# Performance work log

Measured on AMD Instinct MI355X. Metric: run time of the kernel, lower is better.

Reference implementation:

```python
import jax, jax.numpy as jnp
import numpy as np

B, D, CL, QL = 32, 128, 1024, 512


def setup_inputs() -> dict:
    key = jax.random.key(0)
    kC, kQ, kW = jax.random.split(key, 3)
    C = jax.random.normal(kC, (B, D, CL), dtype=jnp.float32)
    Q = jax.random.normal(kQ, (B, D, QL), dtype=jnp.float32)
    # xavier_normal_ on (B*CL, 1, 3D): std = sqrt(2 / (fan_in + fan_out)) = sqrt(2/(1+3D))
    std = (2.0 / (1.0 + 3.0 * D)) ** 0.5
    W = jax.random.normal(kW, (B * CL, 1, 3 * D), dtype=jnp.float32) * std
    return {"C": C, "Q": Q, "W": W}


def reference(C, Q, W):
    # C: (B, D, CL), Q: (B, D, QL), W: (B*CL, 1, 3D)
    b, d, cl = C.shape
    Ct = jnp.transpose(C, (0, 2, 1))   # (B, CL, D)
    Qt = jnp.transpose(Q, (0, 2, 1))   # (B, QL, D)
    Wr = W.reshape(b, cl, 3 * d)
    wq, wc, wqc = Wr[..., :d], Wr[..., d:2 * d], Wr[..., 2 * d:]
    # Trilinear similarity: S[b,c,q] = wq[b,c].Q[b,q] + wc[b,c].C[b,c] + wqc[b,c].(C[b,c]*Q[b,q])
    S = (jnp.einsum('bcd,bqd->bcq', wq, Qt)
         + jnp.sum(wc * Ct, axis=-1, keepdims=True)
         + jnp.einsum('bcd,bqd->bcq', wqc * Ct, Qt))   # (B, CL, QL)
    S1 = jax.nn.softmax(S, axis=2)  # over queries
    S2 = jax.nn.softmax(S, axis=1)  # over context
    A = jnp.einsum('bcq,bqd->bcd', S1, Qt)             # (B, CL, D)
    # B = (S1 @ S2^T) @ C, reassociated as S1 @ (S2^T @ C) to avoid (CL,CL) intermediate
    S2tC = jnp.einsum('bkq,bkd->bqd', S2, Ct)          # (B, QL, D)
    Bm = jnp.einsum('bcq,bqd->bcd', S1, S2tC)          # (B, CL, D)
    out = jnp.concatenate([Ct, A, Ct * A, Ct * Bm], axis=2)  # (B, CL, 4D)
    # dropout is identity in eval mode
    return jnp.transpose(out, (0, 2, 1))               # (B, 4D, CL)
```

## Files before the change

kernel.cpp:

```cpp
#include <hip/hip_runtime.h>
#include <hip/hip_bf16.h>
#include <cstddef>

#define B_  32
#define D_  128
#define CL_ 1024
#define QL_ 512

using short8  = __attribute__((ext_vector_type(8))) short;
using short4v = __attribute__((ext_vector_type(4))) short;
using float4v = __attribute__((ext_vector_type(4))) float;

__device__ __forceinline__ unsigned short f2bf(float f) {
    unsigned int u = __float_as_uint(f);
    u += 0x7FFFu + ((u >> 16) & 1u);
    return (unsigned short)(u >> 16);
}
__device__ __forceinline__ float bf2f(unsigned short h) {
    return __uint_as_float(((unsigned int)h) << 16);
}

__global__ __launch_bounds__(256) void k_u_bias(const float* __restrict__ C,
                                                const float* __restrict__ W,
                                                unsigned short* __restrict__ U,
                                                float* __restrict__ bias,
                                                unsigned short* __restrict__ Cbf) {
    int b  = blockIdx.y;
    int c0 = blockIdx.x * 32;
    int tid = threadIdx.x;

    __shared__ float tile[128][33];
    __shared__ float bred[32][9];

    for (int pass = 0; pass < 16; ++pass) {
        int d = pass * 8 + (tid >> 5);
        int c = tid & 31;
        float v = C[((size_t)(b * D_ + d)) * CL_ + c0 + c];
        tile[d][c] = v;
        Cbf[((size_t)(b * D_ + d)) * CL_ + c0 + c] = f2bf(v);
    }
    __syncthreads();

    int tc    = tid >> 3;
    int lane8 = tid & 7;
    int c     = c0 + tc;
    size_t wbase = ((size_t)(b * CL_ + c)) * (3 * D_);
    size_t ubase = ((size_t)(b * CL_ + c)) * D_;

    float bpart = 0.f;
    #pragma unroll
    for (int i = 0; i < 4; ++i) {
        int d = i * 32 + lane8 * 4;
        float4 wq4  = *(const float4*)(W + wbase + d);
        float4 wc4  = *(const float4*)(W + wbase + D_ + d);
        float4 wqc4 = *(const float4*)(W + wbase + 2 * D_ + d);
        float ct0 = tile[d + 0][tc], ct1 = tile[d + 1][tc];
        float ct2 = tile[d + 2][tc], ct3 = tile[d + 3][tc];
        short4v u;
        u[0] = (short)f2bf(wq4.x + wqc4.x * ct0);
        u[1] = (short)f2bf(wq4.y + wqc4.y * ct1);
        u[2] = (short)f2bf(wq4.z + wqc4.z * ct2);
        u[3] = (short)f2bf(wq4.w + wqc4.w * ct3);
        *(short4v*)(U + ubase + d) = u;
        bpart += wc4.x * ct0 + wc4.y * ct1 + wc4.z * ct2 + wc4.w * ct3;
    }
    bred[tc][lane8] = bpart;
    __syncthreads();
    if (lane8 == 0) {
        float s = 0.f;
        for (int i = 0; i < 8; ++i) s += bred[tc][i];
        bias[b * CL_ + c] = s;
    }
}

__global__ __launch_bounds__(256) void k_qt(const float* __restrict__ Q,
                                            unsigned short* __restrict__ Qt,
                                            unsigned short* __restrict__ Qbf) {
    int b  = blockIdx.z;
    int d0 = blockIdx.y * 64;
    int q0 = blockIdx.x * 64;
    int tid = threadIdx.x;
    __shared__ float t[64][65];
    for (int p = 0; p < 16; ++p) {
        int d = p * 4 + (tid >> 6);
        int q = tid & 63;
        float v = Q[((size_t)(b * D_ + d0 + d)) * QL_ + q0 + q];
        t[d][q] = v;
        Qbf[((size_t)(b * D_ + d0 + d)) * QL_ + q0 + q] = f2bf(v);
    }
    __syncthreads();
    for (int p = 0; p < 16; ++p) {
        int q  = p * 4 + (tid >> 6);
        int dd = tid & 63;
        Qt[((size_t)(b * QL_ + q0 + q)) * D_ + d0 + dd] = f2bf(t[dd][q]);
    }
}

__global__ __launch_bounds__(256) void k_gs2(const unsigned short* __restrict__ Ubf,
                                             const unsigned short* __restrict__ Qtbf,
                                             const float* __restrict__ bias,
                                             unsigned short* __restrict__ Sbf,
                                             float* __restrict__ rmax,
                                             float* __restrict__ rinv,
                                             float* __restrict__ pcmax,
                                             float* __restrict__ pcsum) {
    int mt = blockIdx.x;
    int b  = blockIdx.y;
    int m0 = mt * 64;
    int tid  = threadIdx.x;
    int lane = tid & 63, wave = tid >> 6;
    int wm = wave >> 1, wn = wave & 1;
    int quad = lane >> 4, l15 = lane & 15;

    __shared__ __align__(16) short As[64][136];
    __shared__ __align__(16) short Bs[64][136];
    __shared__ float sbias[64];
    __shared__ float rmw[2][64], rsw[2][64];
    __shared__ float cmw[2][64], csw[2][64];

    const unsigned short* Ab = Ubf  + ((size_t)(b * CL_ + m0)) * D_;
    const unsigned short* Bb = Qtbf + ((size_t)(b * QL_)) * D_;

    #pragma unroll
    for (int i = 0; i < 4; ++i) {
        int flat = tid + i * 256;
        int row = flat >> 4, col = (flat & 15) * 8;
        *(short8*)&As[row][col] = *(const short8*)(Ab + (size_t)row * D_ + col);
    }
    if (tid < 64) sbias[tid] = bias[b * CL_ + m0 + tid];

    float rm_run[2][4], rs_run[2][4];
    #pragma unroll
    for (int fi = 0; fi < 2; ++fi)
        #pragma unroll
        for (int rr = 0; rr < 4; ++rr) { rm_run[fi][rr] = -1e30f; rs_run[fi][rr] = 0.f; }

    for (int chunk = 0; chunk < 8; ++chunk) {
        __syncthreads();
        #pragma unroll
        for (int i = 0; i < 4; ++i) {
            int flat = tid + i * 256;
            int row = flat >> 4, col = (flat & 15) * 8;
            *(short8*)&Bs[row][col] = *(const short8*)(Bb + (size_t)(chunk * 64 + row) * D_ + col);
        }
        __syncthreads();

        float4v acc[2][2] = {};
        #pragma unroll
        for (int ks = 0; ks < 128; ks += 32) {
            short8 af0 = *(const short8*)&As[wm * 32 + l15][ks + quad * 8];
            short8 af1 = *(const short8*)&As[wm * 32 + 16 + l15][ks + quad * 8];
            short8 bf0 = *(const short8*)&Bs[wn * 32 + l15][ks + quad * 8];
            short8 bf1 = *(const short8*)&Bs[wn * 32 + 16 + l15][ks + quad * 8];
            acc[0][0] = __builtin_amdgcn_mfma_f32_16x16x32_bf16(af0, bf0, acc[0][0], 0, 0, 0);
            acc[0][1] = __builtin_amdgcn_mfma_f32_16x16x32_bf16(af0, bf1, acc[0][1], 0, 0, 0);
            acc[1][0] = __builtin_amdgcn_mfma_f32_16x16x32_bf16(af1, bf0, acc[1][0], 0, 0, 0);
            acc[1][1] = __builtin_amdgcn_mfma_f32_16x16x32_bf16(af1, bf1, acc[1][1], 0, 0, 0);
        }

        float v[2][2][4];
        #pragma unroll
        for (int fi = 0; fi < 2; ++fi)
            #pragma unroll
            for (int fj = 0; fj < 2; ++fj)
                #pragma unroll
                for (int rr = 0; rr < 4; ++rr) {
                    int mloc = wm * 32 + fi * 16 + quad * 4 + rr;
                    float x = acc[fi][fj][rr] + sbias[mloc];
                    v[fi][fj][rr] = x;
                    int nloc = wn * 32 + fj * 16 + l15;
                    Sbf[((size_t)(b * CL_ + m0 + mloc)) * QL_ + chunk * 64 + nloc] = f2bf(x);
                }

        #pragma unroll
        for (int fi = 0; fi < 2; ++fi)
            #pragma unroll
            for (int rr = 0; rr < 4; ++rr) {
                float v0 = v[fi][0][rr], v1 = v[fi][1][rr];
                float nm = fmaxf(rm_run[fi][rr], fmaxf(v0, v1));
                rs_run[fi][rr] = rs_run[fi][rr] * __expf(rm_run[fi][rr] - nm)
                               + __expf(v0 - nm) + __expf(v1 - nm);
                rm_run[fi][rr] = nm;
            }

        #pragma unroll
        for (int fj = 0; fj < 2; ++fj) {
            float cm = v[0][fj][0];
            #pragma unroll
            for (int fi = 0; fi < 2; ++fi)
                #pragma unroll
                for (int rr = 0; rr < 4; ++rr) cm = fmaxf(cm, v[fi][fj][rr]);
            float cs = 0.f;
            #pragma unroll
            for (int fi = 0; fi < 2; ++fi)
                #pragma unroll
                for (int rr = 0; rr < 4; ++rr) cs += __expf(v[fi][fj][rr] - cm);
            #pragma unroll
            for (int off = 16; off <= 32; off <<= 1) {
                float om = __shfl_xor(cm, off);
                float os = __shfl_xor(cs, off);
                float nm = fmaxf(cm, om);
                cs = cs * __expf(cm - nm) + os * __expf(om - nm);
                cm = nm;
            }
            if (quad == 0) {
                int col = wn * 32 + fj * 16 + l15;
                cmw[wm][col] = cm;
                csw[wm][col] = cs;
            }
        }
        __syncthreads();
        if (tid < 64) {
            float m0v = cmw[0][tid], s0v = csw[0][tid];
            float m1v = cmw[1][tid], s1v = csw[1][tid];
            float nm = fmaxf(m0v, m1v);
            float ss = s0v * __expf(m0v - nm) + s1v * __expf(m1v - nm);
            size_t pi = ((size_t)(b * 16 + mt)) * QL_ + chunk * 64 + tid;
            pcmax[pi] = nm;
            pcsum[pi] = ss;
        }
    }

    #pragma unroll
    for (int off = 1; off <= 8; off <<= 1)
        #pragma unroll
        for (int fi = 0; fi < 2; ++fi)
            #pragma unroll
            for (int rr = 0; rr < 4; ++rr) {
                float om = __shfl_xor(rm_run[fi][rr], off);
                float os = __shfl_xor(rs_run[fi][rr], off);
                float nm = fmaxf(rm_run[fi][rr], om);
                rs_run[fi][rr] = rs_run[fi][rr] * __expf(rm_run[fi][rr] - nm)
                               + os * __expf(om - nm);
                rm_run[fi][rr] = nm;
            }
    if (l15 == 0) {
        #pragma unroll
        for (int fi = 0; fi < 2; ++fi)
            #pragma unroll
            for (int rr = 0; rr < 4; ++rr) {
                int m = wm * 32 + fi * 16 + quad * 4 + rr;
                rmw[wn][m] = rm_run[fi][rr];
                rsw[wn][m] = rs_run[fi][rr];
            }
    }
    __syncthreads();
    if (tid < 64) {
        float m0v = rmw[0][tid], s0v = rsw[0][tid];
        float m1v = rmw[1][tid], s1v = rsw[1][tid];
        float nm = fmaxf(m0v, m1v);
        float ss = s0v * __expf(m0v - nm) + s1v * __expf(m1v - nm);
        rmax[b * CL_ + m0 + tid] = nm;
        rinv[b * CL_ + m0 + tid] = 1.0f / ss;
    }
}

__global__ __launch_bounds__(256) void k_col_reduce(const float* __restrict__ pcmax,
                                                    const float* __restrict__ pcsum,
                                                    float* __restrict__ cmax,
                                                    float* __restrict__ cinv) {
    int g = blockIdx.x * 256 + threadIdx.x;
    int b = g >> 9, q = g & (QL_ - 1);
    float M = -1e30f, SS = 0.f;
    #pragma unroll
    for (int ch = 0; ch < 16; ++ch) {
        size_t idx = ((size_t)(b * 16 + ch)) * QL_ + q;
        float m = pcmax[idx], s = pcsum[idx];
        float nM = fmaxf(M, m);
        SS = SS * __expf(M - nM) + s * __expf(m - nM);
        M = nM;
    }
    cmax[g] = M;
    cinv[g] = 1.0f / SS;
}

__global__ __launch_bounds__(256) void k_gp(const unsigned short* __restrict__ Cbf,
                                            const unsigned short* __restrict__ Sbf,
                                            const float* __restrict__ cmax,
                                            const float* __restrict__ cinv,
                                            unsigned short* __restrict__ Pbf) {
    int b  = blockIdx.y;
    int q0 = blockIdx.x * 32;

    int tid  = threadIdx.x;
    int lane = tid & 63, wave = tid >> 6;
    int quad = lane >> 4, l15 = lane & 15;

    __shared__ __align__(16) short As[128][72];
    __shared__ __align__(16) short Bs[32][72];
    __shared__ float scm[32], sci[32];

    if (tid < 32) {
        scm[tid] = cmax[b * QL_ + q0 + tid];
        sci[tid] = cinv[b * QL_ + q0 + tid];
    }
    __syncthreads();

    const unsigned short* Cb = Cbf + (size_t)b * D_ * CL_;
    const unsigned short* Sb = Sbf + (size_t)b * CL_ * QL_;

    int arow = tid >> 3;
    int acol = (tid & 7) * 8;
    int srow = tid >> 4;
    int uq   = tid & 15;

    float4v acc[2][2] = {};

    for (int k0 = 0; k0 < CL_; k0 += 64) {
        #pragma unroll
        for (int p = 0; p < 4; ++p) {
            int row = p * 32 + arow;
            *(short8*)&As[row][acol] = *(const short8*)(Cb + (size_t)row * CL_ + k0 + acol);
        }
        #pragma unroll
        for (int p = 0; p < 4; ++p) {
            int crow = p * 16 + srow;
            unsigned int raw = *(const unsigned int*)(Sb + (size_t)(k0 + crow) * QL_ + q0 + 2 * uq);
            float v0 = __expf(bf2f((unsigned short)(raw & 0xFFFF)) - scm[2 * uq]) * sci[2 * uq];
            float v1 = __expf(bf2f((unsigned short)(raw >> 16)) - scm[2 * uq + 1]) * sci[2 * uq + 1];
            Bs[2 * uq][crow]     = (short)f2bf(v0);
            Bs[2 * uq + 1][crow] = (short)f2bf(v1);
        }
        __syncthreads();
        #pragma unroll
        for (int ks = 0; ks < 64; ks += 32) {
            short8 a0 = *(const short8*)&As[wave * 32 + l15][ks + quad * 8];
            short8 a1 = *(const short8*)&As[wave * 32 + 16 + l15][ks + quad * 8];
            short8 b0 = *(const short8*)&Bs[l15][ks + quad * 8];
            short8 b1 = *(const short8*)&Bs[16 + l15][ks + quad * 8];
            acc[0][0] = __builtin_amdgcn_mfma_f32_16x16x32_bf16(a0, b0, acc[0][0], 0, 0, 0);
            acc[0][1] = __builtin_amdgcn_mfma_f32_16x16x32_bf16(a0, b1, acc[0][1], 0, 0, 0);
            acc[1][0] = __builtin_amdgcn_mfma_f32_16x16x32_bf16(a1, b0, acc[1][0], 0, 0, 0);
            acc[1][1] = __builtin_amdgcn_mfma_f32_16x16x32_bf16(a1, b1, acc[1][1], 0, 0, 0);
        }
        __syncthreads();
    }

    #pragma unroll
    for (int fi = 0; fi < 2; ++fi)
        #pragma unroll
        for (int fj = 0; fj < 2; ++fj)
            #pragma unroll
            for (int rr = 0; rr < 4; ++rr) {
                int d = wave * 32 + fi * 16 + quad * 4 + rr;
                int q = q0 + fj * 16 + l15;
                Pbf[((size_t)(b * D_ + d)) * QL_ + q] = f2bf(acc[fi][fj][rr]);
            }
}

template <int PLANE>
__global__ __launch_bounds__(256) void k_av(const unsigned short* __restrict__ A,
                                            const unsigned short* __restrict__ Sbf,
                                            const float* __restrict__ rmax,
                                            const float* __restrict__ rinv,
                                            const float* __restrict__ C,
                                            float* __restrict__ out) {
    int b  = blockIdx.y;
    int n0 = blockIdx.x * 32;

    int tid  = threadIdx.x;
    int lane = tid & 63, wave = tid >> 6;
    int quad = lane >> 4, l15 = lane & 15;

    __shared__ __align__(16) short As[128][72];
    __shared__ __align__(16) short Bs[32][72];
    __shared__ float srm[32], sri[32];

    if (tid < 32) {
        srm[tid] = rmax[b * CL_ + n0 + tid];
        sri[tid] = rinv[b * CL_ + n0 + tid];
    }
    __syncthreads();

    const unsigned short* Ab = A + (size_t)b * D_ * QL_;
    const unsigned short* Sb = Sbf + ((size_t)(b * CL_ + n0)) * QL_;

    int arow = tid >> 3;
    int acol = (tid & 7) * 8;

    float4v acc[2][2] = {};

    for (int k0 = 0; k0 < QL_; k0 += 64) {
        #pragma unroll
        for (int p = 0; p < 4; ++p) {
            int row = p * 32 + arow;
            *(short8*)&As[row][acol] = *(const short8*)(Ab + (size_t)row * QL_ + k0 + acol);
        }
        {
            int brow = tid >> 3;
            uint4 raw = *(const uint4*)(Sb + (size_t)brow * QL_ + k0 + acol);
            unsigned int rw[4] = {raw.x, raw.y, raw.z, raw.w};
            float rm = srm[brow], ri = sri[brow];
            short8 v;
            #pragma unroll
            for (int j = 0; j < 8; ++j) {
                unsigned short bits = (unsigned short)((rw[j >> 1] >> ((j & 1) * 16)) & 0xFFFF);
                v[j] = (short)f2bf(__expf(bf2f(bits) - rm) * ri);
            }
            *(short8*)&Bs[brow][acol] = v;
        }
        __syncthreads();
        #pragma unroll
        for (int ks = 0; ks < 64; ks += 32) {
            short8 a0 = *(const short8*)&As[wave * 32 + l15][ks + quad * 8];
            short8 a1 = *(const short8*)&As[wave * 32 + 16 + l15][ks + quad * 8];
            short8 b0 = *(const short8*)&Bs[l15][ks + quad * 8];
            short8 b1 = *(const short8*)&Bs[16 + l15][ks + quad * 8];
            acc[0][0] = __builtin_amdgcn_mfma_f32_16x16x32_bf16(a0, b0, acc[0][0], 0, 0, 0);
            acc[0][1] = __builtin_amdgcn_mfma_f32_16x16x32_bf16(a0, b1, acc[0][1], 0, 0, 0);
            acc[1][0] = __builtin_amdgcn_mfma_f32_16x16x32_bf16(a1, b0, acc[1][0], 0, 0, 0);
            acc[1][1] = __builtin_amdgcn_mfma_f32_16x16x32_bf16(a1, b1, acc[1][1], 0, 0, 0);
        }
        __syncthreads();
    }

    #pragma unroll
    for (int fi = 0; fi < 2; ++fi)
        #pragma unroll
        for (int fj = 0; fj < 2; ++fj)
            #pragma unroll
            for (int rr = 0; rr < 4; ++rr) {
                int d = wave * 32 + fi * 16 + quad * 4 + rr;
                int c = n0 + fj * 16 + l15;
                float ct = C[((size_t)(b * D_ + d)) * CL_ + c];
                float v  = acc[fi][fj][rr];
                size_t ob = ((size_t)(b * 4 * D_ + d)) * CL_ + c;
                if (PLANE == 0) {
                    out[ob]                        = ct;
                    out[ob + (size_t)D_ * CL_]     = v;
                    out[ob + 2 * (size_t)D_ * CL_] = ct * v;
                } else {
                    out[ob + 3 * (size_t)D_ * CL_] = ct * v;
                }
            }
}

extern "C" void kernel_launch(void* const* d_in, const int* in_sizes, int n_in,
                              void* d_out, int out_size, void* d_ws, size_t ws_size,
                              hipStream_t stream) {
    const float* C = (const float*)d_in[0];
    const float* Q = (const float*)d_in[1];
    const float* W = (const float*)d_in[2];
    float* out = (float*)d_out;

    unsigned short* Ubf  = (unsigned short*)d_ws;
    unsigned short* Qtbf = Ubf  + (size_t)B_ * CL_ * D_;
    unsigned short* Qbf  = Qtbf + (size_t)B_ * QL_ * D_;
    unsigned short* Cbf  = Qbf  + (size_t)B_ * D_ * QL_;
    unsigned short* Pbf  = Cbf  + (size_t)B_ * D_ * CL_;
    unsigned short* Sbf  = Pbf  + (size_t)B_ * D_ * QL_;
    float* bias  = (float*)(Sbf + (size_t)B_ * CL_ * QL_);
    float* rmax  = bias  + (size_t)B_ * CL_;
    float* rinv  = rmax  + (size_t)B_ * CL_;
    float* cmax  = rinv  + (size_t)B_ * CL_;
    float* cinv  = cmax  + (size_t)B_ * QL_;
    float* pcmax = cinv  + (size_t)B_ * QL_;
    float* pcsum = pcmax + (size_t)B_ * 16 * QL_;

    k_u_bias<<<dim3(CL_ / 32, B_), 256, 0, stream>>>(C, W, Ubf, bias, Cbf);
    k_qt<<<dim3(QL_ / 64, D_ / 64, B_), 256, 0, stream>>>(Q, Qtbf, Qbf);
    k_gs2<<<dim3(16, B_), 256, 0, stream>>>(Ubf, Qtbf, bias, Sbf, rmax, rinv, pcmax, pcsum);
    k_col_reduce<<<B_ * QL_ / 256, 256, 0, stream>>>(pcmax, pcsum, cmax, cinv);
    k_gp<<<dim3(QL_ / 32, B_), 256, 0, stream>>>(Cbf, Sbf, cmax, cinv, Pbf);
    k_av<0><<<dim3(CL_ / 32, B_), 256, 0, stream>>>(Qbf, Sbf, rmax, rinv, C, out);
    k_av<1><<<dim3(CL_ / 32, B_), 256, 0, stream>>>(Pbf, Sbf, rmax, rinv, C, out);
}
```

Before: 208.0 us.

## Fuse column-softmax reduce into k_gp and merge two AV kernels into one

The separate column-reduce kernel goes away: k_gp now merges the 16 partial column max/sum chunks itself for its 32 queries. The two k_av launches, which each recomputed the row softmax of S and reread S and C, become one k_av2. It multiplies the same softmax tile against both Q and P with a 64-column tile and 2x2 wave layout, then writes all four output planes. This removes two launches and halves the S reads and exp work in the AV stage, at the cost of more LDS and accumulator registers, which may lower occupancy.

```diff
diff --git a/kernel.cpp b/kernel.cpp
--- a/kernel.cpp
+++ b/kernel.cpp
@@ -255,29 +255,10 @@
     }
 }
 
-__global__ __launch_bounds__(256) void k_col_reduce(const float* __restrict__ pcmax,
-                                                    const float* __restrict__ pcsum,
-                                                    float* __restrict__ cmax,
-                                                    float* __restrict__ cinv) {
-    int g = blockIdx.x * 256 + threadIdx.x;
-    int b = g >> 9, q = g & (QL_ - 1);
-    float M = -1e30f, SS = 0.f;
-    #pragma unroll
-    for (int ch = 0; ch < 16; ++ch) {
-        size_t idx = ((size_t)(b * 16 + ch)) * QL_ + q;
-        float m = pcmax[idx], s = pcsum[idx];
-        float nM = fmaxf(M, m);
-        SS = SS * __expf(M - nM) + s * __expf(m - nM);
-        M = nM;
-    }
-    cmax[g] = M;
-    cinv[g] = 1.0f / SS;
-}
-
 __global__ __launch_bounds__(256) void k_gp(const unsigned short* __restrict__ Cbf,
                                             const unsigned short* __restrict__ Sbf,
-                                            const float* __restrict__ cmax,
-                                            const float* __restrict__ cinv,
+                                            const float* __restrict__ pcmax,
+                                            const float* __restrict__ pcsum,
                                             unsigned short* __restrict__ Pbf) {
     int b  = blockIdx.y;
     int q0 = blockIdx.x * 32;
@@ -291,8 +272,17 @@
     __shared__ float scm[32], sci[32];
 
     if (tid < 32) {
-        scm[tid] = cmax[b * QL_ + q0 + tid];
-        sci[tid] = cinv[b * QL_ + q0 + tid];
+        float M = -1e30f, SS = 0.f;
+        #pragma unroll
+        for (int ch = 0; ch < 16; ++ch) {
+            size_t idx = ((size_t)(b * 16 + ch)) * QL_ + q0 + tid;
+            float m = pcmax[idx], s = pcsum[idx];
+            float nM = fmaxf(M, m);
+            SS = SS * __expf(M - nM) + s * __expf(m - nM);
+            M = nM;
+        }
+        scm[tid] = M;
+        sci[tid] = 1.0f / SS;
     }
     __syncthreads();
 
@@ -348,90 +338,101 @@
             }
 }
 
-template <int PLANE>
-__global__ __launch_bounds__(256) void k_av(const unsigned short* __restrict__ A,
-                                            const unsigned short* __restrict__ Sbf,
-                                            const float* __restrict__ rmax,
-                                            const float* __restrict__ rinv,
-                                            const float* __restrict__ C,
-                                            float* __restrict__ out) {
+__global__ __launch_bounds__(256) void k_av2(const unsigned short* __restrict__ Qbf,
+                                             const unsigned short* __restrict__ Pbf,
+                                             const unsigned short* __restrict__ Sbf,
+                                             const float* __restrict__ rmax,
+                                             const float* __restrict__ rinv,
+                                             const float* __restrict__ C,
+                                             float* __restrict__ out) {
     int b  = blockIdx.y;
-    int n0 = blockIdx.x * 32;
+    int n0 = blockIdx.x * 64;
 
     int tid  = threadIdx.x;
     int lane = tid & 63, wave = tid >> 6;
+    int wm = wave >> 1, wn = wave & 1;
     int quad = lane >> 4, l15 = lane & 15;
 
-    __shared__ __align__(16) short As[128][72];
-    __shared__ __align__(16) short Bs[32][72];
-    __shared__ float srm[32], sri[32];
-
-    if (tid < 32) {
+    __shared__ __align__(16) short AsQ[128][72];
+    __shared__ __align__(16) short AsP[128][72];
+    __shared__ __align__(16) short Bs[64][72];
+    __shared__ float srm[64], sri[64];
+
+    if (tid < 64) {
         srm[tid] = rmax[b * CL_ + n0 + tid];
         sri[tid] = rinv[b * CL_ + n0 + tid];
     }
     __syncthreads();
 
-    const unsigned short* Ab = A + (size_t)b * D_ * QL_;
+    const unsigned short* Qb = Qbf + (size_t)b * D_ * QL_;
+    const unsigned short* Pb = Pbf + (size_t)b * D_ * QL_;
     const unsigned short* Sb = Sbf + ((size_t)(b * CL_ + n0)) * QL_;
 
     int arow = tid >> 3;
     int acol = (tid & 7) * 8;
-
-    float4v acc[2][2] = {};
+    int brow = tid >> 2;
+    int bcol = (tid & 3) * 16;
+    float brm = srm[brow], bri = sri[brow];
+
+    float4v accQ[4][2] = {};
+    float4v accP[4][2] = {};
 
     for (int k0 = 0; k0 < QL_; k0 += 64) {
         #pragma unroll
         for (int p = 0; p < 4; ++p) {
             int row = p * 32 + arow;
-            *(short8*)&As[row][acol] = *(const short8*)(Ab + (size_t)row * QL_ + k0 + acol);
-        }
-        {
-            int brow = tid >> 3;
-            uint4 raw = *(const uint4*)(Sb + (size_t)brow * QL_ + k0 + acol);
+            *(short8*)&AsQ[row][acol] = *(const short8*)(Qb + (size_t)row * QL_ + k0 + acol);
+            *(short8*)&AsP[row][acol] = *(const short8*)(Pb + (size_t)row * QL_ + k0 + acol);
+        }
+        #pragma unroll
+        for (int h = 0; h < 2; ++h) {
+            uint4 raw = *(const uint4*)(Sb + (size_t)brow * QL_ + k0 + bcol + h * 8);
             unsigned int rw[4] = {raw.x, raw.y, raw.z, raw.w};
-            float rm = srm[brow], ri = sri[brow];
             short8 v;
             #pragma unroll
             for (int j = 0; j < 8; ++j) {
                 unsigned short bits = (unsigned short)((rw[j >> 1] >> ((j & 1) * 16)) & 0xFFFF);
-                v[j] = (short)f2bf(__expf(bf2f(bits) - rm) * ri);
-            }
-            *(short8*)&Bs[brow][acol] = v;
+                v[j] = (short)f2bf(__expf(bf2f(bits) - brm) * bri);
+            }
+            *(short8*)&Bs[brow][bcol + h * 8] = v;
         }
         __syncthreads();
         #pragma unroll
         for (int ks = 0; ks < 64; ks += 32) {
-            short8 a0 = *(const short8*)&As[wave * 32 + l15][ks + quad * 8];
-            short8 a1 = *(const short8*)&As[wave * 32 + 16 + l15][ks + quad * 8];
-            short8 b0 = *(const short8*)&Bs[l15][ks + quad * 8];
-            short8 b1 = *(const short8*)&Bs[16 + l15][ks + quad * 8];
-            acc[0][0] = __builtin_amdgcn_mfma_f32_16x16x32_bf16(a0, b0, acc[0][0], 0, 0, 0);
-            acc[0][1] = __builtin_amdgcn_mfma_f32_16x16x32_bf16(a0, b1, acc[0][1], 0, 0, 0);
-            acc[1][0] = __builtin_amdgcn_mfma_f32_16x16x32_bf16(a1, b0, acc[1][0], 0, 0, 0);
-            acc[1][1] = __builtin_amdgcn_mfma_f32_16x16x32_bf16(a1, b1, acc[1][1], 0, 0, 0);
-        }
-        __syncthreads();
-    }
-
-    #pragma unroll
-    for (int fi = 0; fi < 2; ++fi)
+            short8 b0 = *(const short8*)&Bs[wn * 32 + l15][ks + quad * 8];
+            short8 b1 = *(const short8*)&Bs[wn * 32 + 16 + l15][ks + quad * 8];
+            #pragma unroll
+            for (int fi = 0; fi < 4; ++fi) {
+                short8 aq = *(const short8*)&AsQ[wm * 64 + fi * 16 + l15][ks + quad * 8];
+                accQ[fi][0] = __builtin_amdgcn_mfma_f32_16x16x32_bf16(aq, b0, accQ[fi][0], 0, 0, 0);
+                accQ[fi][1] = __builtin_amdgcn_mfma_f32_16x16x32_bf16(aq, b1, accQ[fi][1], 0, 0, 0);
+            }
+            #pragma unroll
+            for (int fi = 0; fi < 4; ++fi) {
+                short8 ap = *(const short8*)&AsP[wm * 64 + fi * 16 + l15][ks + quad * 8];
+                accP[fi][0] = __builtin_amdgcn_mfma_f32_16x16x32_bf16(ap, b0, accP[fi][0], 0, 0, 0);
+                accP[fi][1] = __builtin_amdgcn_mfma_f32_16x16x32_bf16(ap, b1, accP[fi][1], 0, 0, 0);
+            }
+        }
+        __syncthreads();
+    }
+
+    #pragma unroll
+    for (int fi = 0; fi < 4; ++fi)
         #pragma unroll
         for (int fj = 0; fj < 2; ++fj)
             #pragma unroll
             for (int rr = 0; rr < 4; ++rr) {
-                int d = wave * 32 + fi * 16 + quad * 4 + rr;
-                int c = n0 + fj * 16 + l15;
+                int d = wm * 64 + fi * 16 + quad * 4 + rr;
+                int c = n0 + wn * 32 + fj * 16 + l15;
                 float ct = C[((size_t)(b * D_ + d)) * CL_ + c];
-                float v  = acc[fi][fj][rr];
+                float vq = accQ[fi][fj][rr];
+                float vp = accP[fi][fj][rr];
                 size_t ob = ((size_t)(b * 4 * D_ + d)) * CL_ + c;
-                if (PLANE == 0) {
-                    out[ob]                        = ct;
-                    out[ob + (size_t)D_ * CL_]     = v;
-                    out[ob + 2 * (size_t)D_ * CL_] = ct * v;
-                } else {
-                    out[ob + 3 * (size_t)D_ * CL_] = ct * v;
-                }
+                out[ob]                        = ct;
+                out[ob + (size_t)D_ * CL_]     = vq;
+                out[ob + 2 * (size_t)D_ * CL_] = ct * vq;
+                out[ob + 3 * (size_t)D_ * CL_] = ct * vp;
             }
 }
 
@@ -452,16 +453,12 @@
     float* bias  = (float*)(Sbf + (size_t)B_ * CL_ * QL_);
     float* rmax  = bias  + (size_t)B_ * CL_;
     float* rinv  = rmax  + (size_t)B_ * CL_;
-    float* cmax  = rinv  + (size_t)B_ * CL_;
-    float* cinv  = cmax  + (size_t)B_ * QL_;
-    float* pcmax = cinv  + (size_t)B_ * QL_;
+    float* pcmax = rinv  + (size_t)B_ * CL_;
     float* pcsum = pcmax + (size_t)B_ * 16 * QL_;
 
     k_u_bias<<<dim3(CL_ / 32, B_), 256, 0, stream>>>(C, W, Ubf, bias, Cbf);
     k_qt<<<dim3(QL_ / 64, D_ / 64, B_), 256, 0, stream>>>(Q, Qtbf, Qbf);
     k_gs2<<<dim3(16, B_), 256, 0, stream>>>(Ubf, Qtbf, bias, Sbf, rmax, rinv, pcmax, pcsum);
-    k_col_reduce<<<B_ * QL_ / 256, 256, 0, stream>>>(pcmax, pcsum, cmax, cinv);
-    k_gp<<<dim3(QL_ / 32, B_), 256, 0, stream>>>(Cbf, Sbf, cmax, cinv, Pbf);
-    k_av<0><<<dim3(CL_ / 32, B_), 256, 0, stream>>>(Qbf, Sbf, rmax, rinv, C, out);
-    k_av<1><<<dim3(CL_ / 32, B_), 256, 0, stream>>>(Pbf, Sbf, rmax, rinv, C, out);
-}
+    k_gp<<<dim3(QL_ / 32, B_), 256, 0, stream>>>(Cbf, Sbf, pcmax, pcsum, Pbf);
+    k_av2<<<dim3(CL_ / 64, B_), 256, 0, stream>>>(Qbf, Pbf, Sbf, rmax, rinv, C, out);
+}
```

After: 200.3 us. -3.7%, faster.
